# Kernel optimization log

Measured on AMD Instinct MI355X. Metric: run time of the kernel, lower is better.

Reference implementation:

```python
import math
import jax, jax.numpy as jnp
import numpy as np

NUM_HEADS = 8
TEMPORAL_DECAY = 0.1


def setup_inputs() -> dict:
    key = jax.random.key(0)
    ks = jax.random.split(key, 12)
    B, N, D = 2, 2048, 512
    H = NUM_HEADS
    s = 0.02
    inp = {
        "node_features": jax.random.normal(ks[0], (B, N, D), dtype=jnp.float32),
        "adjacency": jax.random.randint(ks[1], (B, N, N), 0, 2, dtype=jnp.int32),
        "edge_times": jax.random.uniform(ks[2], (B, N, N), dtype=jnp.float32),
        "current_time": 2,
        "wq": jax.random.normal(ks[3], (D, D), dtype=jnp.float32) * s,
        "bq": jnp.zeros((D,), dtype=jnp.float32),
        "wk": jax.random.normal(ks[4], (D, D), dtype=jnp.float32) * s,
        "bk": jnp.zeros((D,), dtype=jnp.float32),
        "wv": jax.random.normal(ks[5], (D, D), dtype=jnp.float32) * s,
        "bv": jnp.zeros((D,), dtype=jnp.float32),
        "wo": jax.random.normal(ks[6], (D, D), dtype=jnp.float32) * s,
        "bo": jnp.zeros((D,), dtype=jnp.float32),
        "wt": jax.random.normal(ks[7], (H, 1), dtype=jnp.float32) * s,  # time_proj: Linear(1, H)
        "bt": jnp.zeros((H,), dtype=jnp.float32),
    }
    return inp


def reference(node_features, adjacency, edge_times, current_time,
              wq, bq, wk, bk, wv, bv, wo, bo, wt, bt):
    B, N, D = node_features.shape
    H = NUM_HEADS
    dk = D // H

    def proj(w, b):
        # (B,N,D) -> (B,H,N,dk)
        return (node_features @ w.T + b).reshape(B, N, H, dk).transpose(0, 2, 1, 3)

    q = proj(wq, bq)
    k = proj(wk, bk)
    v = proj(wv, bv)

    # scaled dot-product scores: (B,H,N,N)
    attn = jnp.einsum("bhnd,bhmd->bhnm", q, k) / math.sqrt(dk)

    # adjacency mask (zero entries -> -inf)
    graph_mask = (adjacency == 0)[:, None, :, :]  # (B,1,N,N)
    attn = jnp.where(graph_mask, -jnp.inf, attn)

    # temporal-decay bias: Linear(1, H) applied to exp(-decay * dt), permuted to (B,H,N,N)
    time_diff = jnp.maximum(jnp.float32(current_time) - edge_times, 0.0)  # (B,N,N)
    temporal_weight = jnp.exp(-TEMPORAL_DECAY * time_diff)  # (B,N,N)
    temporal_bias = (temporal_weight[:, None, :, :] * wt[:, 0][None, :, None, None]
                     + bt[None, :, None, None])  # (B,H,N,N)
    attn = attn + temporal_bias

    attn = jax.nn.softmax(attn, axis=-1)  # dropout rate is 0.0

    out = jnp.einsum("bhnm,bhmd->bhnd", attn, v)  # (B,H,N,dk)
    out = out.transpose(0, 2, 1, 3).reshape(B, N, D)
    out = out @ wo.T + bo
    return node_features + out
```

## Files before the change

### kernel.cpp

```cpp
#include <hip/hip_runtime.h>

#define BB 2
#define NN 2048
#define DD 512
#define HH 8
#define DK 64

#define LOG2E 1.44269504f
#define SCL2  0.18033688f

typedef __attribute__((ext_vector_type(4))) float f32x4;
typedef __attribute__((ext_vector_type(16))) float f32x16;
typedef __attribute__((ext_vector_type(8))) short bf16x8;
typedef __attribute__((ext_vector_type(2))) int i32x2;
typedef __attribute__((ext_vector_type(4))) int i32x4;

__device__ __forceinline__ short f2bf(float f) {
  union { float f; unsigned u; } v; v.f = f;
  unsigned r = v.u + 0x7fffu + ((v.u >> 16) & 1u);
  return (short)(r >> 16);
}

__device__ __forceinline__ bf16x8 pack8(float4 a, float4 b) {
  bf16x8 r;
  r[0] = f2bf(a.x); r[1] = f2bf(a.y); r[2] = f2bf(a.z); r[3] = f2bf(a.w);
  r[4] = f2bf(b.x); r[5] = f2bf(b.y); r[6] = f2bf(b.z); r[7] = f2bf(b.w);
  return r;
}

#define WAITV(n) do { asm volatile("s_waitcnt vmcnt(" #n ")" ::: "memory"); \
                      __builtin_amdgcn_sched_barrier(0); } while (0)
#define GLOAD_LDS(g, l) __builtin_amdgcn_global_load_lds( \
    (const __attribute__((address_space(1))) void*)(g),   \
    (__attribute__((address_space(3))) void*)(l), 16, 0, 0)
#define SBAR() asm volatile("s_barrier" ::: "memory")
#define LDM(d, o) asm volatile("global_load_dwordx2 %0, %1, off offset:" o \
                               : "=v"(d) : "v"(mrowp))
#define CVTPK(d, a, b) asm("v_cvt_pk_bf16_f32 %0, %1, %2" : "=v"(d) : "v"(a), "v"(b))
#define PLSWAP(a, b) asm("v_permlane32_swap_b32 %0, %1" : "+v"(a), "+v"(b))

__global__ __launch_bounds__(256) void mask_pre(
    const int* __restrict__ adj, const float* __restrict__ et,
    const int* __restrict__ ctp, short* __restrict__ M)
{
  const float ct = (float)(*ctp);
  const float kd = -0.1f * LOG2E;
  const size_t total = (size_t)BB * NN * NN;
  const size_t stride = (size_t)gridDim.x * 256 * 8;
  for (size_t i = ((size_t)blockIdx.x * 256 + threadIdx.x) * 8; i < total; i += stride) {
    int4 a0 = *(const int4*)(adj + i);
    int4 a1 = *(const int4*)(adj + i + 4);
    float4 e0 = *(const float4*)(et + i);
    float4 e1 = *(const float4*)(et + i + 4);
    const int av[8] = {a0.x, a0.y, a0.z, a0.w, a1.x, a1.y, a1.z, a1.w};
    const float ev[8] = {e0.x, e0.y, e0.z, e0.w, e1.x, e1.y, e1.z, e1.w};
    bf16x8 r;
#pragma unroll
    for (int j = 0; j < 8; j++) {
      const float tv = (av[j] == 0) ? -1.f : exp2f(kd * fmaxf(ct - ev[j], 0.f));
      r[j] = f2bf(tv);
    }
    *(bf16x8*)(M + i) = r;
  }
}

__global__ __launch_bounds__(256) void cast_pre(
    const float* __restrict__ X,
    const float* __restrict__ wq, const float* __restrict__ wk,
    const float* __restrict__ wv, const float* __restrict__ wo,
    short* __restrict__ Xb, short* __restrict__ Wb)
{
  const size_t XN = (size_t)4096 * DD;
  const size_t i = ((size_t)blockIdx.x * 256 + threadIdx.x) * 8;
  const float* src;
  short* dst;
  if (i < XN) { src = X + i; dst = Xb + i; }
  else {
    const size_t j = i - XN;
    const int sel = (int)(j >> 18);
    const size_t off = j & 262143;
    src = (sel == 0 ? wq : sel == 1 ? wk : sel == 2 ? wv : wo) + off;
    dst = Wb + j;
  }
  float4 a = *(const float4*)src;
  float4 b = *(const float4*)(src + 4);
  *(bf16x8*)dst = pack8(a, b);
}

__global__ __launch_bounds__(256, 2) void qkv_gemm(
    const short* __restrict__ Xb, const short* __restrict__ Wb,
    const float* __restrict__ bq, const float* __restrict__ bk, const float* __restrict__ bv,
    short* __restrict__ qo, short* __restrict__ ko, short* __restrict__ vto)
{
  __shared__ short As[2][128 * 64];
  __shared__ short Bs[2][64 * 64];

  const int tid = threadIdx.x;
  const int lane = tid & 63;
  const int w = tid >> 6;
  const int q4 = lane >> 4;
  const int c = lane & 15;

  const int bid = blockIdx.x;
  const int mt = bid & 31;
  const int nt = bid >> 5;
  const int sel = nt >> 3;
  const int nw = (nt & 7) * 64;
  const int m0 = mt * 128;
  const short* Wm = Wb + (size_t)sel * 262144;
  const float* bias = sel == 0 ? bq : (sel == 1 ? bk : bv);
  const float oscale = (sel == 0) ? SCL2 : 1.0f;

  const int sr = lane >> 3;
  const int sc = ((lane & 7) ^ sr) * 8;
  const short* ap = Xb + (size_t)(m0 + w * 32 + sr) * DD + sc;
  const short* bp = Wm + (size_t)(nw + w * 16 + sr) * DD + sc;

  f32x4 acc[2][4];
#pragma unroll
  for (int is = 0; is < 2; is++)
#pragma unroll
    for (int ns = 0; ns < 4; ns++) acc[is][ns] = f32x4{0.f, 0.f, 0.f, 0.f};

#define QSTAGE(BUF, K0)                                                    \
  { GLOAD_LDS(ap + (K0),           &As[BUF][(w * 32 + 0) * 64]);           \
    GLOAD_LDS(ap + 8 * DD + (K0),  &As[BUF][(w * 32 + 8) * 64]);           \
    GLOAD_LDS(ap + 16 * DD + (K0), &As[BUF][(w * 32 + 16) * 64]);          \
    GLOAD_LDS(ap + 24 * DD + (K0), &As[BUF][(w * 32 + 24) * 64]);          \
    GLOAD_LDS(bp + (K0),           &Bs[BUF][(w * 16 + 0) * 64]);           \
    GLOAD_LDS(bp + 8 * DD + (K0),  &Bs[BUF][(w * 16 + 8) * 64]); }

#define QCOMPUTE(BUF)                                                            \
  { const short* Asb = &As[BUF][0];                                              \
    const short* Bsb = &Bs[BUF][0];                                              \
    _Pragma("unroll") for (int kc = 0; kc < 2; kc++) {                           \
      bf16x8 af[2], bfr[4];                                                      \
      _Pragma("unroll") for (int is = 0; is < 2; is++)                           \
        af[is] = *(const bf16x8*)&Asb[(w * 32 + is * 16 + c) * 64 +              \
                                      (((kc * 4 + q4) ^ (c & 7)) * 8)];          \
      _Pragma("unroll") for (int ns = 0; ns < 4; ns++)                           \
        bfr[ns] = *(const bf16x8*)&Bsb[(ns * 16 + c) * 64 +                      \
                                       (((kc * 4 + q4) ^ (c & 7)) * 8)];         \
      _Pragma("unroll") for (int is = 0; is < 2; is++)                           \
        _Pragma("unroll") for (int ns = 0; ns < 4; ns++)                         \
          acc[is][ns] = __builtin_amdgcn_mfma_f32_16x16x32_bf16(af[is], bfr[ns], \
                                                           acc[is][ns], 0, 0, 0); \
    } }

  QSTAGE(0, 0)
  __syncthreads();
  for (int ks = 0; ks < 8; ks++) {
    if (ks < 7) QSTAGE((ks + 1) & 1, (ks + 1) * 64)
    QCOMPUTE(ks & 1)
    __syncthreads();
  }
#undef QSTAGE
#undef QCOMPUTE

#pragma unroll
  for (int ns = 0; ns < 4; ns++) {
    const int n = nw + ns * 16 + c;
    const float bval = bias[n];
    const int hh = n >> 6, d = n & 63;
#pragma unroll
    for (int is = 0; is < 2; is++)
#pragma unroll
      for (int r = 0; r < 4; r++) {
        const int m = m0 + w * 32 + is * 16 + q4 * 4 + r;
        const int bb = m >> 11, tok = m & 2047;
        const float val = (acc[is][ns][r] + bval) * oscale;
        if (sel == 2)      vto[((size_t)(bb * HH + hh) * DK + d) * NN + tok] = f2bf(val);
        else if (sel == 1) ko [((size_t)(bb * HH + hh) * NN + tok) * DK + d] = f2bf(val);
        else               qo [((size_t)(bb * HH + hh) * NN + tok) * DK + d] = f2bf(val);
      }
  }
}

__global__ __launch_bounds__(512, 2) void attn_kernel(
    const short* __restrict__ qt, const short* __restrict__ kt, const short* __restrict__ vtt,
    const short* __restrict__ M,
    const float* __restrict__ wt,
    short* __restrict__ po_out, float* __restrict__ pl_out)
{
  __shared__ short Ks[2][64 * 64];
  __shared__ short Vs[2][64 * 64];

  const int tid = threadIdx.x;
  const int lane = tid & 63;
  const int w = tid >> 6;
  const int l31 = lane & 31;
  const int hi = lane >> 5;

  const int bid = blockIdx.x;
  const int xcd = bid & 7;
  const int b = xcd >> 2;
  const int jsp = xcd & 3;
  const int rest = bid >> 3;
  const int h = rest & 7;
  const int qblk = rest >> 3;
  const int i0w = qblk * 256 + w * 32;
  const int jbase = jsp * 512;

  const float wth2 = wt[h] * LOG2E;

  const short* qb = qt + ((size_t)(b * HH + h) * NN + i0w) * DK;
  const short* kb = kt + (size_t)(b * HH + h) * NN * DK;
  const short* vb = vtt + (size_t)(b * HH + h) * DK * NN;
  const short* mrowp = M + ((size_t)b * NN + i0w + l31) * NN + jbase + hi * 4;

  bf16x8 aq[4];
#pragma unroll
  for (int kc = 0; kc < 4; kc++)
    aq[kc] = *(const bf16x8*)(qb + l31 * DK + kc * 16 + hi * 8);
  asm volatile("" :: "v"(aq[0]), "v"(aq[1]), "v"(aq[2]), "v"(aq[3]), "v"(wth2));
  WAITV(0);

  float lp = 0.f;
  f32x16 oacc[2];
#pragma unroll
  for (int ds = 0; ds < 2; ds++)
#pragma unroll
    for (int r = 0; r < 16; r++) oacc[ds][r] = 0.f;

  const short* kp = kb + (size_t)(jbase + w * 8 + (lane >> 3)) * DK + ((lane & 7) ^ (lane >> 3)) * 8;
  const short* vp = vb + (size_t)(w * 8 + (lane >> 3)) * NN + jbase + ((lane & 7) ^ (lane >> 3)) * 8;
  short* Ksb0 = &Ks[0][0];
  short* Vsb0 = &Vs[0][0];

#define STAGE(BUFN)                                                        \
  { GLOAD_LDS(kp, Ksb0 + (BUFN) * 4096 + w * 512);                         \
    GLOAD_LDS(vp, Vsb0 + (BUFN) * 4096 + w * 512);                         \
    __builtin_amdgcn_sched_barrier(0); }

#define KADV() { kp += 64 * DK; vp += 64; }
#define MADV() { mrowp += 64; }

#define ISSUE_MASK(MU)                                                     \
  { LDM(MU[0][0], "0");  LDM(MU[0][1], "16"); LDM(MU[0][2], "32");  LDM(MU[0][3], "48");  \
    LDM(MU[1][0], "64"); LDM(MU[1][1], "80"); LDM(MU[1][2], "96");  LDM(MU[1][3], "112"); \
    __builtin_amdgcn_sched_barrier(0); }

  i32x2 muA[2][4], muB[2][4];

  STAGE(0)
  KADV()
  ISSUE_MASK(muA)
  MADV()

#define COMPUTE_QK(BUFC)                                                         \
    const short* Ksb = Ksb0 + (BUFC) * 4096;                                     \
    const short* Vsb = Vsb0 + (BUFC) * 4096;                                     \
    f32x16 sacc[2];                                                              \
    __builtin_amdgcn_s_setprio(1);                                               \
    _Pragma("unroll") for (int js = 0; js < 2; js++) {                           \
      _Pragma("unroll") for (int r = 0; r < 16; r++) sacc[js][r] = 0.f;          \
      _Pragma("unroll") for (int kc = 0; kc < 4; kc++) {                         \
        bf16x8 kf = *(const bf16x8*)&Ksb[(js * 32 + l31) * 64 +                  \
                                         (((kc * 2 + hi) ^ (l31 & 7)) * 8)];     \
        sacc[js] = __builtin_amdgcn_mfma_f32_32x32x16_bf16(kf, aq[kc],           \
                                                           sacc[js], 0, 0, 0);   \
      }                                                                          \
    }                                                                            \
    __builtin_amdgcn_s_setprio(0);

#define COMPUTE_SM_PV(MU)                                                        \
    __builtin_amdgcn_s_setprio(1);                                               \
    _Pragma("unroll") for (int js = 0; js < 2; js++) {                           \
      float p[16];                                                               \
      _Pragma("unroll") for (int r = 0; r < 16; r++) {                           \
        const int dw = ((r & 3) < 2) ? MU[js][r >> 2][0] : MU[js][r >> 2][1];    \
        union { float f; unsigned u; } tu;                                       \
        tu.u = (r & 1) ? ((unsigned)dw & 0xffff0000u) : ((unsigned)dw << 16);    \
        const float tv = tu.f;                                                   \
        const float pp = exp2f(fmaf(tv, wth2, sacc[js][r]));                     \
        p[r] = (tv < 0.f) ? 0.f : pp;                                            \
        lp += p[r];                                                              \
      }                                                                          \
      bf16x8 pf[2];                                                              \
      _Pragma("unroll") for (int ch = 0; ch < 2; ch++) {                         \
        const int rb = ch * 8;                                                   \
        int w0, w1, w2, w3;                                                      \
        CVTPK(w0, p[rb + 0], p[rb + 1]);                                         \
        CVTPK(w1, p[rb + 2], p[rb + 3]);                                         \
        CVTPK(w2, p[rb + 4], p[rb + 5]);                                         \
        CVTPK(w3, p[rb + 6], p[rb + 7]);                                         \
        PLSWAP(w0, w2);                      \
        PLSWAP(w1, w3);                                                          \
        i32x4 bi;                                                                \
        bi[0] = w0; bi[1] = w1; bi[2] = w2; bi[3] = w3;                          \
        union { i32x4 i; bf16x8 h; } cv; cv.i = bi;                              \
        pf[ch] = cv.h;                                                           \
      }                                                                          \
      _Pragma("unroll") for (int ds = 0; ds < 2; ds++) {                         \
        _Pragma("unroll") for (int ch = 0; ch < 2; ch++) {                       \
          bf16x8 vf = *(const bf16x8*)&Vsb[(ds * 32 + l31) * 64 +                \
                         (((js * 4 + ch * 2 + hi) ^ (l31 & 7)) * 8)];            \
          oacc[ds] = __builtin_amdgcn_mfma_f32_32x32x16_bf16(vf, pf[ch],         \
                                                             oacc[ds], 0, 0, 0); \
        }                                                                        \
      }                                                                          \
    }                                                                            \
    __builtin_amdgcn_s_setprio(0);

#define ATTN_ITER(T, MUC, MUN)                                                   \
  {                                                                              \
    STAGE(((T) + 1) & 1)                        \
    KADV()                                                                       \
    WAITV(10);                                   \
    SBAR();                                                                      \
    COMPUTE_QK((T) & 1)                                                          \
    ISSUE_MASK(MUN)                             \
    MADV()                                                                       \
    WAITV(10);                                   \
    COMPUTE_SM_PV(MUC)                                                           \
    SBAR();                                                                      \
  }

  for (int t2 = 0; t2 < 3; t2++) {
    ATTN_ITER(2 * t2,     muA, muB)
    ATTN_ITER(2 * t2 + 1, muB, muA)
  }
  ATTN_ITER(6, muA, muB)
  {
    WAITV(8);
    SBAR();
    COMPUTE_QK(1)
    WAITV(0);
    COMPUTE_SM_PV(muB)
  }

#undef ATTN_ITER
#undef COMPUTE_QK
#undef COMPUTE_SM_PV
#undef STAGE
#undef KADV
#undef MADV
#undef ISSUE_MASK

  const float lt = lp + __shfl_xor(lp, 32);
  const size_t ridx = ((size_t)(jsp * BB + b) * HH + h) * NN + i0w + l31;
  if (lane < 32) pl_out[ridx] = lt;
  short* pob = po_out + ridx * DK;
#pragma unroll
  for (int ds = 0; ds < 2; ds++)
#pragma unroll
    for (int r = 0; r < 16; r++) {
      const int d = ds * 32 + (r & 3) + 8 * (r >> 2) + 4 * hi;
      pob[d] = f2bf(oacc[ds][r]);
    }
}

__global__ __launch_bounds__(256) void combine(
    const short* __restrict__ PO, const float* __restrict__ PL,
    short* __restrict__ AO)
{
  const int g = blockIdx.x * 256 + threadIdx.x;
  const int t8 = g & 7;
  const int h  = (g >> 3) & 7;
  const int n  = (g >> 6) & 2047;
  const int b  = g >> 17;
  float acc[8] = {0.f, 0.f, 0.f, 0.f, 0.f, 0.f, 0.f, 0.f};
  float ls = 0.f;
#pragma unroll
  for (int jp = 0; jp < 4; jp++) {
    const size_t ridx = ((size_t)(jp * BB + b) * HH + h) * NN + n;
    bf16x8 v = *(const bf16x8*)(PO + ridx * DK + t8 * 8);
    ls += PL[ridx];
#pragma unroll
    for (int e = 0; e < 8; e++) {
      union { float f; unsigned u; } cv;
      cv.u = ((unsigned)(unsigned short)v[e]) << 16;
      acc[e] += cv.f;
    }
  }
  const float rl = 1.0f / ls;
  bf16x8 o;
#pragma unroll
  for (int e = 0; e < 8; e++) o[e] = f2bf(acc[e] * rl);
  *(bf16x8*)(AO + (size_t)g * 8) = o;
}

__global__ __launch_bounds__(256, 2) void out_gemm(
    const short* __restrict__ AO, const short* __restrict__ wob, const float* __restrict__ bo,
    const float* __restrict__ nf, float* __restrict__ out)
{
  __shared__ short As[2][128 * 64];
  __shared__ short Bs[2][64 * 64];

  const int tid = threadIdx.x;
  const int lane = tid & 63;
  const int w = tid >> 6;
  const int q4 = lane >> 4;
  const int c = lane & 15;

  const int bid = blockIdx.x;
  const int mt = bid & 31;
  const int n0 = (bid >> 5) * 64;
  const int m0 = mt * 128;

  const int sr = lane >> 3;
  const int sc = ((lane & 7) ^ sr) * 8;
  const short* ap = AO + (size_t)(m0 + w * 32 + sr) * DD + sc;
  const short* bp = wob + (size_t)(n0 + w * 16 + sr) * DD + sc;

  f32x4 acc[2][4];
#pragma unroll
  for (int is = 0; is < 2; is++)
#pragma unroll
    for (int ns = 0; ns < 4; ns++) acc[is][ns] = f32x4{0.f, 0.f, 0.f, 0.f};

#define OSTAGE(BUF, K0)                                                    \
  { GLOAD_LDS(ap + (K0),           &As[BUF][(w * 32 + 0) * 64]);           \
    GLOAD_LDS(ap + 8 * DD + (K0),  &As[BUF][(w * 32 + 8) * 64]);           \
    GLOAD_LDS(ap + 16 * DD + (K0), &As[BUF][(w * 32 + 16) * 64]);          \
    GLOAD_LDS(ap + 24 * DD + (K0), &As[BUF][(w * 32 + 24) * 64]);          \
    GLOAD_LDS(bp + (K0),           &Bs[BUF][(w * 16 + 0) * 64]);           \
    GLOAD_LDS(bp + 8 * DD + (K0),  &Bs[BUF][(w * 16 + 8) * 64]); }

#define OCOMPUTE(BUF)                                                            \
  { const short* Asb = &As[BUF][0];                                              \
    const short* Bsb = &Bs[BUF][0];                                              \
    _Pragma("unroll") for (int kc = 0; kc < 2; kc++) {                           \
      bf16x8 af[2], bfr[4];                                                      \
      _Pragma("unroll") for (int is = 0; is < 2; is++)                           \
        af[is] = *(const bf16x8*)&Asb[(w * 32 + is * 16 + c) * 64 +              \
                                      (((kc * 4 + q4) ^ (c & 7)) * 8)];          \
      _Pragma("unroll") for (int ns = 0; ns < 4; ns++)                           \
        bfr[ns] = *(const bf16x8*)&Bsb[(ns * 16 + c) * 64 +                      \
                                       (((kc * 4 + q4) ^ (c & 7)) * 8)];         \
      _Pragma("unroll") for (int is = 0; is < 2; is++)                           \
        _Pragma("unroll") for (int ns = 0; ns < 4; ns++)                         \
          acc[is][ns] = __builtin_amdgcn_mfma_f32_16x16x32_bf16(af[is], bfr[ns], \
                                                           acc[is][ns], 0, 0, 0); \
    } }

  OSTAGE(0, 0)
  __syncthreads();
  for (int ks = 0; ks < 8; ks++) {
    if (ks < 7) OSTAGE((ks + 1) & 1, (ks + 1) * 64)
    OCOMPUTE(ks & 1)
    __syncthreads();
  }
#undef OSTAGE
#undef OCOMPUTE

#pragma unroll
  for (int ns = 0; ns < 4; ns++) {
    const int n = n0 + ns * 16 + c;
    const float bval = bo[n];
#pragma unroll
    for (int is = 0; is < 2; is++)
#pragma unroll
      for (int r = 0; r < 4; r++) {
        const int m = m0 + w * 32 + is * 16 + q4 * 4 + r;
        out[(size_t)m * DD + n] = acc[is][ns][r] + bval + nf[(size_t)m * DD + n];
      }
  }
}

extern "C" void kernel_launch(void* const* d_in, const int* in_sizes, int n_in,
                              void* d_out, int out_size, void* d_ws, size_t ws_size,
                              hipStream_t stream) {
  const float* nf  = (const float*)d_in[0];
  const int*   adj = (const int*)d_in[1];
  const float* et  = (const float*)d_in[2];
  const int*   ct  = (const int*)d_in[3];
  const float* wq  = (const float*)d_in[4];
  const float* bq  = (const float*)d_in[5];
  const float* wk  = (const float*)d_in[6];
  const float* bk  = (const float*)d_in[7];
  const float* wv  = (const float*)d_in[8];
  const float* bv  = (const float*)d_in[9];
  const float* wo  = (const float*)d_in[10];
  const float* bo  = (const float*)d_in[11];
  const float* wt  = (const float*)d_in[12];

  const size_t SZ = (size_t)BB * HH * NN * DK;
  short* q   = (short*)d_ws;
  short* k   = q + SZ;
  short* vt  = k + SZ;
  short* ao  = vt + SZ;
  short* Mm  = ao + SZ;
  short* PO  = Mm + (size_t)BB * NN * NN;
  float* PL  = (float*)(PO + 4 * SZ);
  short* Xb  = (short*)(PL + 4 * BB * HH * NN);
  short* Wb  = Xb + (size_t)4096 * DD;

  cast_pre<<<1536, 256, 0, stream>>>(nf, wq, wk, wv, wo, Xb, Wb);
  mask_pre<<<2048, 256, 0, stream>>>(adj, et, ct, Mm);
  qkv_gemm<<<768, 256, 0, stream>>>(Xb, Wb, bq, bk, bv, q, k, vt);
  attn_kernel<<<512, 512, 0, stream>>>(q, k, vt, Mm, wt, PO, PL);
  combine<<<1024, 256, 0, stream>>>(PO, PL, ao);
  out_gemm<<<256, 256, 0, stream>>>(ao, Wb + 3 * 262144, bo, nf, (float*)d_out);
}
```

Before: 103.5 us.

## Merge prep kernels and halve attention block size to 4 waves

Fuses the cast and mask preprocessing kernels into one launch. The attention kernel now runs 1024 blocks of 4 waves each, where it previously ran 512 blocks of 8 waves, so each wave stages 16 K/V rows per tile instead of 8 and the wait counts change to match. LDS fragment addresses are precomputed as byte offsets per lane. The goal is to cut launch overhead and improve scheduling granularity and occupancy. The cost is a higher per-wave staging load and smaller K/V sharing per block.

New measurement: 97.30 us, median of 2. 6.0% less time.

```diff
diff --git a/kernel.cpp b/kernel.cpp
--- a/kernel.cpp
+++ b/kernel.cpp
@@ -39,15 +39,21 @@
 #define CVTPK(d, a, b) asm("v_cvt_pk_bf16_f32 %0, %1, %2" : "=v"(d) : "v"(a), "v"(b))
 #define PLSWAP(a, b) asm("v_permlane32_swap_b32 %0, %1" : "+v"(a), "+v"(b))
 
-__global__ __launch_bounds__(256) void mask_pre(
+__global__ __launch_bounds__(256) void prep(
     const int* __restrict__ adj, const float* __restrict__ et,
-    const int* __restrict__ ctp, short* __restrict__ M)
+    const int* __restrict__ ctp, short* __restrict__ M,
+    const float* __restrict__ X,
+    const float* __restrict__ wq, const float* __restrict__ wk,
+    const float* __restrict__ wv, const float* __restrict__ wo,
+    short* __restrict__ Xb, short* __restrict__ Wb)
 {
   const float ct = (float)(*ctp);
   const float kd = -0.1f * LOG2E;
-  const size_t total = (size_t)BB * NN * NN;
-  const size_t stride = (size_t)gridDim.x * 256 * 8;
-  for (size_t i = ((size_t)blockIdx.x * 256 + threadIdx.x) * 8; i < total; i += stride) {
+  const size_t base = ((size_t)blockIdx.x * 256 + threadIdx.x) * 8;
+  const size_t stride = (size_t)2048 * 256 * 8;
+#pragma unroll
+  for (int it = 0; it < 2; it++) {
+    const size_t i = base + (size_t)it * stride;
     int4 a0 = *(const int4*)(adj + i);
     int4 a1 = *(const int4*)(adj + i + 4);
     float4 e0 = *(const float4*)(et + i);
@@ -62,29 +68,23 @@
     }
     *(bf16x8*)(M + i) = r;
   }
-}
-
-__global__ __launch_bounds__(256) void cast_pre(
-    const float* __restrict__ X,
-    const float* __restrict__ wq, const float* __restrict__ wk,
-    const float* __restrict__ wv, const float* __restrict__ wo,
-    short* __restrict__ Xb, short* __restrict__ Wb)
-{
-  const size_t XN = (size_t)4096 * DD;
-  const size_t i = ((size_t)blockIdx.x * 256 + threadIdx.x) * 8;
-  const float* src;
-  short* dst;
-  if (i < XN) { src = X + i; dst = Xb + i; }
-  else {
-    const size_t j = i - XN;
-    const int sel = (int)(j >> 18);
-    const size_t off = j & 262143;
-    src = (sel == 0 ? wq : sel == 1 ? wk : sel == 2 ? wv : wo) + off;
-    dst = Wb + j;
-  }
-  float4 a = *(const float4*)src;
-  float4 b = *(const float4*)(src + 4);
-  *(bf16x8*)dst = pack8(a, b);
+  if (blockIdx.x < 1536) {
+    const size_t XN = (size_t)4096 * DD;
+    const size_t i = base;
+    const float* src;
+    short* dst;
+    if (i < XN) { src = X + i; dst = Xb + i; }
+    else {
+      const size_t j = i - XN;
+      const int sel = (int)(j >> 18);
+      const size_t off = j & 262143;
+      src = (sel == 0 ? wq : sel == 1 ? wk : sel == 2 ? wv : wo) + off;
+      dst = Wb + j;
+    }
+    float4 a = *(const float4*)src;
+    float4 b = *(const float4*)(src + 4);
+    *(bf16x8*)dst = pack8(a, b);
+  }
 }
 
 __global__ __launch_bounds__(256, 2) void qkv_gemm(
@@ -176,7 +176,7 @@
   }
 }
 
-__global__ __launch_bounds__(512, 2) void attn_kernel(
+__global__ __launch_bounds__(256, 2) void attn_kernel(
     const short* __restrict__ qt, const short* __restrict__ kt, const short* __restrict__ vtt,
     const short* __restrict__ M,
     const float* __restrict__ wt,
@@ -190,6 +190,7 @@
   const int w = tid >> 6;
   const int l31 = lane & 31;
   const int hi = lane >> 5;
+  const int l7 = l31 & 7;
 
   const int bid = blockIdx.x;
   const int xcd = bid & 7;
@@ -198,7 +199,7 @@
   const int rest = bid >> 3;
   const int h = rest & 7;
   const int qblk = rest >> 3;
-  const int i0w = qblk * 256 + w * 32;
+  const int i0w = qblk * 128 + w * 32;
   const int jbase = jsp * 512;
 
   const float wth2 = wt[h] * LOG2E;
@@ -215,6 +216,16 @@
   asm volatile("" :: "v"(aq[0]), "v"(aq[1]), "v"(aq[2]), "v"(aq[3]), "v"(wth2));
   WAITV(0);
 
+  unsigned ka[4], va[4];
+#pragma unroll
+  for (int kc = 0; kc < 4; kc++)
+    ka[kc] = (unsigned)(l31 * 128 + (((kc * 2 + hi) ^ l7) * 16));
+#pragma unroll
+  for (int jc = 0; jc < 4; jc++) {
+    const int js = jc >> 1, ch = jc & 1;
+    va[jc] = (unsigned)(l31 * 128 + (((js * 4 + ch * 2 + hi) ^ l7) * 16));
+  }
+
   float lp = 0.f;
   f32x16 oacc[2];
 #pragma unroll
@@ -222,17 +233,23 @@
 #pragma unroll
     for (int r = 0; r < 16; r++) oacc[ds][r] = 0.f;
 
-  const short* kp = kb + (size_t)(jbase + w * 8 + (lane >> 3)) * DK + ((lane & 7) ^ (lane >> 3)) * 8;
-  const short* vp = vb + (size_t)(w * 8 + (lane >> 3)) * NN + jbase + ((lane & 7) ^ (lane >> 3)) * 8;
-  short* Ksb0 = &Ks[0][0];
-  short* Vsb0 = &Vs[0][0];
+  const int srow = lane >> 3;
+  const int ssw = ((lane & 7) ^ srow) * 8;
+  const short* kp0 = kb + (size_t)(jbase + w * 16 + srow) * DK + ssw;
+  const short* kp1 = kp0 + 8 * DK;
+  const short* vp0 = vb + (size_t)(w * 16 + srow) * NN + jbase + ssw;
+  const short* vp1 = vp0 + 8 * NN;
+  const char* KsB = (const char*)&Ks[0][0];
+  const char* VsB = (const char*)&Vs[0][0];
 
 #define STAGE(BUFN)                                                        \
-  { GLOAD_LDS(kp, Ksb0 + (BUFN) * 4096 + w * 512);                         \
-    GLOAD_LDS(vp, Vsb0 + (BUFN) * 4096 + w * 512);                         \
+  { GLOAD_LDS(kp0, &Ks[BUFN][(w * 16) * 64]);                              \
+    GLOAD_LDS(kp1, &Ks[BUFN][(w * 16 + 8) * 64]);                          \
+    GLOAD_LDS(vp0, &Vs[BUFN][(w * 16) * 64]);                              \
+    GLOAD_LDS(vp1, &Vs[BUFN][(w * 16 + 8) * 64]);                          \
     __builtin_amdgcn_sched_barrier(0); }
 
-#define KADV() { kp += 64 * DK; vp += 64; }
+#define KADV() { kp0 += 64 * DK; kp1 += 64 * DK; vp0 += 64; vp1 += 64; }
 #define MADV() { mrowp += 64; }
 
 #define ISSUE_MASK(MU)                                                     \
@@ -248,22 +265,19 @@
   MADV()
 
 #define COMPUTE_QK(BUFC)                                                         \
-    const short* Ksb = Ksb0 + (BUFC) * 4096;                                     \
-    const short* Vsb = Vsb0 + (BUFC) * 4096;                                     \
     f32x16 sacc[2];                                                              \
     __builtin_amdgcn_s_setprio(1);                                               \
     _Pragma("unroll") for (int js = 0; js < 2; js++) {                           \
       _Pragma("unroll") for (int r = 0; r < 16; r++) sacc[js][r] = 0.f;          \
       _Pragma("unroll") for (int kc = 0; kc < 4; kc++) {                         \
-        bf16x8 kf = *(const bf16x8*)&Ksb[(js * 32 + l31) * 64 +                  \
-                                         (((kc * 2 + hi) ^ (l31 & 7)) * 8)];     \
+        bf16x8 kf = *(const bf16x8*)(KsB + (BUFC) * 8192 + js * 4096 + ka[kc]);  \
         sacc[js] = __builtin_amdgcn_mfma_f32_32x32x16_bf16(kf, aq[kc],           \
                                                            sacc[js], 0, 0, 0);   \
       }                                                                          \
     }                                                                            \
     __builtin_amdgcn_s_setprio(0);
 
-#define COMPUTE_SM_PV(MU)                                                        \
+#define COMPUTE_SM_PV(BUFC, MU)                                                  \
     __builtin_amdgcn_s_setprio(1);                                               \
     _Pragma("unroll") for (int js = 0; js < 2; js++) {                           \
       float p[16];                                                               \
@@ -284,7 +298,7 @@
         CVTPK(w1, p[rb + 2], p[rb + 3]);                                         \
         CVTPK(w2, p[rb + 4], p[rb + 5]);                                         \
         CVTPK(w3, p[rb + 6], p[rb + 7]);                                         \
-        PLSWAP(w0, w2);                      \
+        PLSWAP(w0, w2);                                                          \
         PLSWAP(w1, w3);                                                          \
         i32x4 bi;                                                                \
         bi[0] = w0; bi[1] = w1; bi[2] = w2; bi[3] = w3;                          \
@@ -293,8 +307,8 @@
       }                                                                          \
       _Pragma("unroll") for (int ds = 0; ds < 2; ds++) {                         \
         _Pragma("unroll") for (int ch = 0; ch < 2; ch++) {                       \
-          bf16x8 vf = *(const bf16x8*)&Vsb[(ds * 32 + l31) * 64 +                \
-                         (((js * 4 + ch * 2 + hi) ^ (l31 & 7)) * 8)];            \
+          bf16x8 vf = *(const bf16x8*)(VsB + (BUFC) * 8192 + ds * 4096 +         \
+                                       va[js * 2 + ch]);                         \
           oacc[ds] = __builtin_amdgcn_mfma_f32_32x32x16_bf16(vf, pf[ch],         \
                                                              oacc[ds], 0, 0, 0); \
         }                                                                        \
@@ -306,13 +320,13 @@
   {                                                                              \
     STAGE(((T) + 1) & 1)                        \
     KADV()                                                                       \
-    WAITV(10);                                   \
+    WAITV(12);                                   \
     SBAR();                                                                      \
     COMPUTE_QK((T) & 1)                                                          \
     ISSUE_MASK(MUN)                             \
     MADV()                                                                       \
-    WAITV(10);                                   \
-    COMPUTE_SM_PV(MUC)                                                           \
+    WAITV(12);                                   \
+    COMPUTE_SM_PV((T) & 1, MUC)                                                  \
     SBAR();                                                                      \
   }
 
@@ -326,7 +340,7 @@
     SBAR();
     COMPUTE_QK(1)
     WAITV(0);
-    COMPUTE_SM_PV(muB)
+    COMPUTE_SM_PV(1, muB)
   }
 
 #undef ATTN_ITER
@@ -486,10 +500,9 @@
   short* Xb  = (short*)(PL + 4 * BB * HH * NN);
   short* Wb  = Xb + (size_t)4096 * DD;
 
-  cast_pre<<<1536, 256, 0, stream>>>(nf, wq, wk, wv, wo, Xb, Wb);
-  mask_pre<<<2048, 256, 0, stream>>>(adj, et, ct, Mm);
+  prep<<<2048, 256, 0, stream>>>(adj, et, ct, Mm, nf, wq, wk, wv, wo, Xb, Wb);
   qkv_gemm<<<768, 256, 0, stream>>>(Xb, Wb, bq, bk, bv, q, k, vt);
-  attn_kernel<<<512, 512, 0, stream>>>(q, k, vt, Mm, wt, PO, PL);
+  attn_kernel<<<1024, 256, 0, stream>>>(q, k, vt, Mm, wt, PO, PL);
   combine<<<1024, 256, 0, stream>>>(PO, PL, ao);
   out_gemm<<<256, 256, 0, stream>>>(ao, Wb + 3 * 262144, bo, nf, (float*)d_out);
 }
```
